# Kernel tuning notes

Measured on AMD Instinct MI355X. Metric: run time of the kernel, lower is better.

Reference implementation:

```python
import jax, jax.numpy as jnp
import numpy as np
import math

N = 50000      # nodes
E = 800000     # edges (avg degree 16)
T = 4          # time steps
F = 64         # feature dim (in = hidden = out)
MAX_LEN = 200  # positional encoding table length
EPS = 1e-5     # BatchNorm eps


def _make_pe(time_dim, max_len):
    pe = np.zeros((max_len, time_dim), dtype=np.float32)
    position = np.arange(max_len, dtype=np.float32)[:, None]
    div_term = np.exp(np.arange(0, time_dim, 2, dtype=np.float32) * (-math.log(10000.0) / time_dim))
    pe[:, 0::2] = np.sin(position * div_term)
    pe[:, 1::2] = np.cos(position * div_term)
    return jnp.asarray(pe)


def setup_inputs() -> dict:
    key = jax.random.key(0)
    ks = jax.random.split(key, 10)
    xav = math.sqrt(2.0 / (F + F))  # xavier_normal_ std for square linear
    return {
        "node_features": jax.random.normal(ks[0], (N, T, F), dtype=jnp.float32),
        "edges_weight": jax.random.uniform(ks[1], (T, E), dtype=jnp.float32),
        "identities": jax.random.randint(ks[2], (T,), 0, MAX_LEN),
        "edge_src": jax.random.randint(ks[3], (E,), 0, N),
        "edge_dst": jax.random.randint(ks[4], (E,), 0, N),
        "pe": _make_pe(F, MAX_LEN),
        "W0": jax.random.normal(ks[5], (F, F), dtype=jnp.float32) * xav,
        "W1": jax.random.normal(ks[6], (F, F), dtype=jnp.float32) * xav,
        "g0": jnp.ones((F,), jnp.float32),
        "b0": jnp.zeros((F,), jnp.float32),
        "g1": jnp.ones((F,), jnp.float32),
        "b1": jnp.zeros((F,), jnp.float32),
    }


def _gcn_layer(h, ew, edge_src, edge_dst, W):
    # gather-mul-scatter: msg_e = h[src_e] * w_e ; agg_v = sum_{e: dst=v} msg_e
    msg = h[edge_src] * ew                                   # (E, T, F)
    agg = jax.ops.segment_sum(msg, edge_dst, num_segments=N)  # (N, T, F)
    readout = agg.mean(axis=0)                                # dgl.mean_nodes (single graph) -> (T, F)
    return agg @ W, readout @ W


def _batchnorm(x, gamma, beta):
    # training-mode batch stats over all non-channel dims
    mean = x.mean(axis=(0, 1))
    var = x.var(axis=(0, 1))
    return (x - mean) * jax.lax.rsqrt(var + EPS) * gamma + beta


def reference(node_features, edges_weight, identities, edge_src, edge_dst,
              pe, W0, W1, g0, b0, g1, b1):
    # positional encoding added per time step
    h = node_features + pe[identities]          # (N, T, F)
    ew = edges_weight.T[:, :, None]             # (E, T, 1)
    # layer 0: gcn -> dropout(eval=identity) -> BN -> ReLU
    h, readout = _gcn_layer(h, ew, edge_src, edge_dst, W0)
    h = jax.nn.relu(_batchnorm(h, g0, b0))
    # layer 1 (output layer)
    h, readout = _gcn_layer(h, ew, edge_src, edge_dst, W1)
    h = jax.nn.relu(_batchnorm(h, g1, b1))
    return h, readout
```

## Files before the change

kernel.cpp:

```cpp
#include <hip/hip_runtime.h>

#define TF 256

typedef __attribute__((ext_vector_type(8))) short short8;
typedef __attribute__((ext_vector_type(4))) float f32x4;
typedef __attribute__((ext_vector_type(4))) unsigned int uint4v;
typedef __attribute__((ext_vector_type(2))) unsigned int uint2v;

__device__ inline unsigned short f2bf(float x) {
  unsigned u = __float_as_uint(x);
  u += 0x7fffu + ((u >> 16) & 1u);
  return (unsigned short)(u >> 16);
}
__device__ inline unsigned pack2(unsigned short lo, unsigned short hi) {
  return (unsigned)lo | ((unsigned)hi << 16);
}
__device__ inline float bflo(unsigned u) { return __uint_as_float(u << 16); }
__device__ inline float bfhi(unsigned u) { return __uint_as_float(u & 0xffff0000u); }

__global__ void prep_hist_kernel(const float* __restrict__ x, const float* __restrict__ pe,
                                 const int* __restrict__ ids, uint2v* __restrict__ h0, int n4,
                                 const int* __restrict__ dst, int* __restrict__ indeg, int E) {
  const int gid = blockIdx.x * blockDim.x + threadIdx.x;
  const int stride = gridDim.x * blockDim.x;
  for (int i = gid; i < n4; i += stride) {
    int e0 = (i << 2) & (TF - 1);
    int t = e0 >> 6;
    int f4 = e0 & 63;
    f32x4 v = __builtin_nontemporal_load(&reinterpret_cast<const f32x4*>(x)[i]);
    const f32x4 p = *reinterpret_cast<const f32x4*>(&pe[ids[t] * 64 + f4]);
    uint2v o;
    o.x = pack2(f2bf(v.x + p.x), f2bf(v.y + p.y));
    o.y = pack2(f2bf(v.z + p.z), f2bf(v.w + p.w));
    h0[i] = o;
  }
  for (int e = gid; e < E; e += stride) {
    atomicAdd(&indeg[__builtin_nontemporal_load(&dst[e])], 1);
  }
}

__global__ __launch_bounds__(1024) void scan_part1(const int* __restrict__ indeg,
                                                   int* __restrict__ partials, int n) {
  __shared__ int wsum[16];
  const int tid = threadIdx.x;
  const int lane = tid & 63;
  const int wid = tid >> 6;
  int i = blockIdx.x * 1024 + tid;
  int s = (i < n) ? indeg[i] : 0;
  #pragma unroll
  for (int o = 1; o < 64; o <<= 1) s += __shfl_xor(s, o, 64);
  if (lane == 0) wsum[wid] = s;
  __syncthreads();
  if (tid == 0) {
    int acc = 0;
    #pragma unroll
    for (int w = 0; w < 16; ++w) acc += wsum[w];
    partials[blockIdx.x] = acc;
  }
}

__global__ __launch_bounds__(512) void scan2_wfrag_kernel(
    const int* __restrict__ partials, int* __restrict__ base, int* __restrict__ offsets,
    int nb, int n, const float* __restrict__ W0, const float* __restrict__ W1,
    short* __restrict__ wf0, short* __restrict__ wf1) {
  const int tid = threadIdx.x;
  if (tid < 64) {
    int v = (tid < nb) ? partials[tid] : 0;
    int s = v;
    #pragma unroll
    for (int o = 1; o < 64; o <<= 1) {
      int t = __shfl_up(s, o, 64);
      if (tid >= o) s += t;
    }
    if (tid < nb) base[tid] = s - v;
    if (tid == nb - 1) offsets[n] = s;
  }
  const int frag = tid >> 6, lane = tid & 63;
  const int c = frag >> 1, h = frag & 1;
  const int col = (c << 4) + (lane & 15);
  const int k0 = h * 32 + ((lane >> 4) << 3);
  short* o0 = wf0 + frag * 512 + lane * 8;
  short* o1 = wf1 + frag * 512 + lane * 8;
  #pragma unroll
  for (int i = 0; i < 8; ++i) {
    o0[i] = (short)f2bf(W0[(k0 + i) * 64 + col]);
    o1[i] = (short)f2bf(W1[(k0 + i) * 64 + col]);
  }
}

__global__ __launch_bounds__(1024) void scan_part3(const int* __restrict__ indeg,
                                                   const int* __restrict__ base,
                                                   int* __restrict__ offsets,
                                                   int* __restrict__ cursor, int n) {
  __shared__ int wsum[16];
  const int tid = threadIdx.x;
  const int lane = tid & 63;
  const int wid = tid >> 6;
  int i = blockIdx.x * 1024 + tid;
  int v = (i < n) ? indeg[i] : 0;
  int s = v;
  #pragma unroll
  for (int o = 1; o < 64; o <<= 1) {
    int t = __shfl_up(s, o, 64);
    if (lane >= o) s += t;
  }
  if (lane == 63) wsum[wid] = s;
  __syncthreads();
  if (tid == 0) {
    int acc = 0;
    #pragma unroll
    for (int w = 0; w < 16; ++w) { int t = wsum[w]; wsum[w] = acc; acc += t; }
  }
  __syncthreads();
  int excl = s - v + wsum[wid] + base[blockIdx.x];
  if (i < n) { offsets[i] = excl; cursor[i] = excl; }
}

__global__ void fill_kernel(const int* __restrict__ src, const int* __restrict__ dst,
                            const float* __restrict__ ew, int* __restrict__ cursor,
                            uint4v* __restrict__ csr_ent, int E) {
  int e = blockIdx.x * blockDim.x + threadIdx.x;
  if (e >= E) return;
  int d = __builtin_nontemporal_load(&dst[e]);
  int pos = atomicAdd(&cursor[d], 1);
  uint4v ent;
  ent.x = (unsigned)(__builtin_nontemporal_load(&src[e]) << 9);
  float w0 = __builtin_nontemporal_load(&ew[e]);
  float w1 = __builtin_nontemporal_load(&ew[(size_t)E + e]);
  float w2 = __builtin_nontemporal_load(&ew[2 * (size_t)E + e]);
  float w3 = __builtin_nontemporal_load(&ew[3 * (size_t)E + e]);
  ent.y = pack2(f2bf(w0), f2bf(w1));
  ent.z = pack2(f2bf(w2), f2bf(w3));
  ent.w = 0u;
  __builtin_nontemporal_store(ent, &csr_ent[pos]);
}

template <int LAYER>
__global__ __launch_bounds__(256) void aggregate_kernel(
    const char* __restrict__ h_base, const int* __restrict__ offsets,
    const uint4v* __restrict__ csr_ent,
    const float* __restrict__ red, const float* __restrict__ g,
    const float* __restrict__ b, float inv_count,
    uint4v* __restrict__ agg, int n_nodes) {
  __shared__ float s_sc[64], s_sh[64];
  const int tid = threadIdx.x;
  if (LAYER == 1) {
    if (tid < 64) {
      float sum = red[tid] + red[64 + tid] + red[128 + tid] + red[192 + tid];
      float mean = sum * inv_count;
      float var = red[256 + tid] * inv_count - mean * mean;
      float sc = g[tid] * rsqrtf(var + 1e-5f);
      s_sc[tid] = sc;
      s_sh[tid] = fmaf(-mean, sc, b[tid]);
    }
    __syncthreads();
  }
  const int lane = tid & 63;
  const int wid = tid >> 6;
  const int v = blockIdx.x * 4 + wid;
  if (v >= n_nodes) return;
  const int p = lane >> 5;
  const unsigned q = lane & 31;
  const unsigned qb = q << 4;
  const int tw = q >> 3;

  float sc[8], sh[8];
  if (LAYER == 1) {
    const int f0 = (q & 7) << 3;
    #pragma unroll
    for (int j = 0; j < 8; ++j) { sc[j] = s_sc[f0 + j]; sh[j] = s_sh[f0 + j]; }
  }

  float acc[8];
  #pragma unroll
  for (int j = 0; j < 8; ++j) acc[j] = 0.f;

  auto wext = [&](uint4v ent) -> float {
    unsigned word = (tw & 2) ? ent.z : ent.y;
    return (tw & 1) ? bfhi(word) : bflo(word);
  };
  auto body = [&](uint4v u, float w) {
    float x[8] = {bflo(u.x), bfhi(u.x), bflo(u.y), bfhi(u.y),
                  bflo(u.z), bfhi(u.z), bflo(u.w), bfhi(u.w)};
    #pragma unroll
    for (int j = 0; j < 8; ++j) {
      float t = x[j];
      if (LAYER == 1) t = fmaxf(0.f, fmaf(t, sc[j], sh[j]));
      acc[j] = fmaf(w, t, acc[j]);
    }
  };

  const int beg = offsets[v];
  const int end = offsets[v + 1];
  int i = beg;
  for (; i + 8 <= end; i += 8) {
    uint4v ent[4];
    #pragma unroll
    for (int c = 0; c < 4; ++c) ent[c] = csr_ent[i + 2 * c + p];
    uint4v row[4];
    #pragma unroll
    for (int c = 0; c < 4; ++c)
      row[c] = *reinterpret_cast<const uint4v*>(h_base + (ent[c].x + qb));
    #pragma unroll
    for (int c = 0; c < 4; ++c) body(row[c], wext(ent[c]));
  }
  for (; i + 2 <= end; i += 2) {
    const uint4v ent = csr_ent[i + p];
    const uint4v row = *reinterpret_cast<const uint4v*>(h_base + (ent.x + qb));
    body(row, wext(ent));
  }
  if (i < end) {
    const uint4v ent = csr_ent[i];
    const uint4v row = *reinterpret_cast<const uint4v*>(h_base + (ent.x + qb));
    body(row, p == 0 ? wext(ent) : 0.f);
  }

  #pragma unroll
  for (int j = 0; j < 8; ++j) acc[j] += __shfl_xor(acc[j], 32, 64);
  if (lane < 32) {
    uint4v o;
    o.x = pack2(f2bf(acc[0]), f2bf(acc[1]));
    o.y = pack2(f2bf(acc[2]), f2bf(acc[3]));
    o.z = pack2(f2bf(acc[4]), f2bf(acc[5]));
    o.w = pack2(f2bf(acc[6]), f2bf(acc[7]));
    __builtin_nontemporal_store(o, &agg[(size_t)v * 32 + q]);
  }
}

__global__ __launch_bounds__(256) void mfma_matmul_kernel(
    const unsigned short* __restrict__ aggb, const short* __restrict__ wf,
    unsigned short* __restrict__ y_bf, float* __restrict__ part, int R) {
  const int tid = threadIdx.x;
  const int lane = tid & 63;
  const int wid = tid >> 6;

  short8 bfr[8];
  #pragma unroll
  for (int g = 0; g < 8; ++g)
    bfr[g] = *reinterpret_cast<const short8*>(wf + g * 512 + lane * 8);

  f32x4 csum[4];
  float ssq[4];
  #pragma unroll
  for (int c = 0; c < 4; ++c) { csum[c] = (f32x4){0.f, 0.f, 0.f, 0.f}; ssq[c] = 0.f; }

  const int nrb = (R + 15) >> 4;
  const int k0 = (lane >> 4) << 3;
  for (int rb = blockIdx.x * 4 + wid; rb < nrb; rb += gridDim.x * 4) {
    const int base = rb << 4;
    const int row = base + (lane & 15);
    short8 a0 = (short8){0, 0, 0, 0, 0, 0, 0, 0};
    short8 a1 = a0;
    if (row < R) {
      const short8* ap = reinterpret_cast<const short8*>(aggb + (size_t)row * 64 + k0);
      a0 = __builtin_nontemporal_load(ap);
      a1 = __builtin_nontemporal_load(ap + 4);
    }
    f32x4 acc[4];
    #pragma unroll
    for (int c = 0; c < 4; ++c) {
      acc[c] = (f32x4){0.f, 0.f, 0.f, 0.f};
      acc[c] = __builtin_amdgcn_mfma_f32_16x16x32_bf16(a0, bfr[c * 2 + 0], acc[c], 0, 0, 0);
      acc[c] = __builtin_amdgcn_mfma_f32_16x16x32_bf16(a1, bfr[c * 2 + 1], acc[c], 0, 0, 0);
    }
    const int rbase = base + ((lane >> 4) << 2);
    #pragma unroll
    for (int c = 0; c < 4; ++c) {
      const int col = (c << 4) + (lane & 15);
      #pragma unroll
      for (int i = 0; i < 4; ++i) {
        const int r2 = rbase + i;
        if (r2 < R) {
          const float val = acc[c][i];
          y_bf[(size_t)r2 * 64 + col] = f2bf(val);
          csum[c][i] += val;
          ssq[c] += val * val;
        }
      }
    }
  }

  #pragma unroll
  for (int c = 0; c < 4; ++c) {
    #pragma unroll
    for (int i = 0; i < 4; ++i) {
      float v = csum[c][i];
      v += __shfl_xor(v, 16, 64);
      v += __shfl_xor(v, 32, 64);
      csum[c][i] = v;
    }
    float q = ssq[c];
    q += __shfl_xor(q, 16, 64);
    q += __shfl_xor(q, 32, 64);
    ssq[c] = q;
  }
  __shared__ float lcs[4][256];
  __shared__ float lsq[4][64];
  if (lane < 16) {
    #pragma unroll
    for (int c = 0; c < 4; ++c) {
      #pragma unroll
      for (int i = 0; i < 4; ++i) lcs[wid][i * 64 + (c << 4) + lane] = csum[c][i];
      lsq[wid][(c << 4) + lane] = ssq[c];
    }
  }
  __syncthreads();
  float s = lcs[0][tid] + lcs[1][tid] + lcs[2][tid] + lcs[3][tid];
  part[(size_t)blockIdx.x * 320 + tid] = s;
  if (tid < 64)
    part[(size_t)blockIdx.x * 320 + 256 + tid] =
        lsq[0][tid] + lsq[1][tid] + lsq[2][tid] + lsq[3][tid];
}

__global__ __launch_bounds__(1024) void reduce_part_kernel(const float* __restrict__ part,
                                                           float* __restrict__ red, int nblk) {
  __shared__ float lds[1024];
  const int tid = threadIdx.x;
  const int col = blockIdx.x * 16 + (tid & 15);
  const int r = tid >> 4;
  float s = 0.f;
  for (int bk = r; bk < nblk; bk += 64) s += part[(size_t)bk * 320 + col];
  lds[tid] = s;
  __syncthreads();
  #pragma unroll
  for (int off = 512; off >= 16; off >>= 1) {
    if (tid < off) lds[tid] += lds[tid + off];
    __syncthreads();
  }
  if (tid < 16) red[col] = lds[tid];
}

__global__ __launch_bounds__(256) void bn_relu_out_kernel(
    const uint4v* __restrict__ yb, const float* __restrict__ red,
    const float* __restrict__ g, const float* __restrict__ b, float inv_count,
    float* __restrict__ out_readout, float invN, f32x4* __restrict__ out, int n8) {
  __shared__ float s_sc[64], s_sh[64];
  const int tid = threadIdx.x;
  if (tid < 64) {
    float sum = red[tid] + red[64 + tid] + red[128 + tid] + red[192 + tid];
    float mean = sum * inv_count;
    float var = red[256 + tid] * inv_count - mean * mean;
    float sc = g[tid] * rsqrtf(var + 1e-5f);
    s_sc[tid] = sc;
    s_sh[tid] = fmaf(-mean, sc, b[tid]);
  }
  __syncthreads();
  if (blockIdx.x == 0) out_readout[tid] = red[tid] * invN;
  const int i = blockIdx.x * 256 + tid;
  if (i >= n8) return;
  const int f0 = (i & 7) << 3;
  uint4v u = __builtin_nontemporal_load(&yb[i]);
  float x[8] = {bflo(u.x), bfhi(u.x), bflo(u.y), bfhi(u.y),
                bflo(u.z), bfhi(u.z), bflo(u.w), bfhi(u.w)};
  f32x4 o0, o1;
  o0.x = fmaxf(0.f, fmaf(x[0], s_sc[f0 + 0], s_sh[f0 + 0]));
  o0.y = fmaxf(0.f, fmaf(x[1], s_sc[f0 + 1], s_sh[f0 + 1]));
  o0.z = fmaxf(0.f, fmaf(x[2], s_sc[f0 + 2], s_sh[f0 + 2]));
  o0.w = fmaxf(0.f, fmaf(x[3], s_sc[f0 + 3], s_sh[f0 + 3]));
  o1.x = fmaxf(0.f, fmaf(x[4], s_sc[f0 + 4], s_sh[f0 + 4]));
  o1.y = fmaxf(0.f, fmaf(x[5], s_sc[f0 + 5], s_sh[f0 + 5]));
  o1.z = fmaxf(0.f, fmaf(x[6], s_sc[f0 + 6], s_sh[f0 + 6]));
  o1.w = fmaxf(0.f, fmaf(x[7], s_sc[f0 + 7], s_sh[f0 + 7]));
  __builtin_nontemporal_store(o0, &out[i * 2 + 0]);
  __builtin_nontemporal_store(o1, &out[i * 2 + 1]);
}

extern "C" void kernel_launch(void* const* d_in, const int* in_sizes, int n_in,
                              void* d_out, int out_size, void* d_ws, size_t ws_size,
                              hipStream_t stream) {
  const float* node_features = (const float*)d_in[0];
  const float* edges_weight  = (const float*)d_in[1];
  const int*   identities    = (const int*)d_in[2];
  const int*   edge_src      = (const int*)d_in[3];
  const int*   edge_dst      = (const int*)d_in[4];
  const float* pe            = (const float*)d_in[5];
  const float* W0            = (const float*)d_in[6];
  const float* W1            = (const float*)d_in[7];
  const float* g0            = (const float*)d_in[8];
  const float* b0            = (const float*)d_in[9];
  const float* g1            = (const float*)d_in[10];
  const float* b1            = (const float*)d_in[11];

  const int T = in_sizes[2];
  const int E = in_sizes[3];
  const int F = in_sizes[8];
  const int N = in_sizes[0] / (T * F);
  const int R = N * T;

  float* out = (float*)d_out;
  float* out_h = out;
  float* out_readout = out + (size_t)N * T * F;

  char* ws = (char*)d_ws;
  size_t off = 0;
  auto alloc = [&](size_t bytes) -> void* {
    off = (off + 255) & ~(size_t)255;
    void* p = ws + off;
    off += bytes;
    return p;
  };
  int*    indeg    = (int*)alloc((size_t)N * sizeof(int));
  int*    partials = (int*)alloc(64 * sizeof(int));
  int*    base_    = (int*)alloc(64 * sizeof(int));
  int*    offsets  = (int*)alloc(((size_t)N + 1) * sizeof(int));
  int*    cursor   = (int*)alloc((size_t)N * sizeof(int));
  uint4v* csr_ent  = (uint4v*)alloc(((size_t)E + 16) * 16);
  unsigned short* h0b  = (unsigned short*)alloc((size_t)N * TF * 2);
  unsigned short* aggb = (unsigned short*)alloc((size_t)N * TF * 2);
  short* wf0 = (short*)alloc(8 * 512 * sizeof(short));
  short* wf1 = (short*)alloc(8 * 512 * sizeof(short));
  const int MMB = 512;
  float* mm_part = (float*)alloc((size_t)MMB * 320 * sizeof(float));
  float* red     = (float*)alloc(320 * sizeof(float));
  (void)ws_size;

  const int nb = (N + 1023) / 1024;
  const float invR = 1.0f / (float)R;

  (void)hipMemsetAsync(indeg, 0, (size_t)N * sizeof(int), stream);
  hipLaunchKernelGGL(prep_hist_kernel, dim3(2048), dim3(256), 0, stream,
                     node_features, pe, identities, (uint2v*)h0b, (N * TF) / 4,
                     edge_dst, indeg, E);
  hipLaunchKernelGGL(scan_part1, dim3(nb), dim3(1024), 0, stream, indeg, partials, N);
  hipLaunchKernelGGL(scan2_wfrag_kernel, dim3(1), dim3(512), 0, stream,
                     partials, base_, offsets, nb, N, W0, W1, wf0, wf1);
  hipLaunchKernelGGL(scan_part3, dim3(nb), dim3(1024), 0, stream, indeg, base_, offsets, cursor, N);
  hipLaunchKernelGGL(fill_kernel, dim3((E + 255) / 256), dim3(256), 0, stream,
                     edge_src, edge_dst, edges_weight, cursor, csr_ent, E);

  const int agg_blocks = (N + 3) / 4;

  hipLaunchKernelGGL((aggregate_kernel<0>), dim3(agg_blocks), dim3(256), 0, stream,
                     (const char*)h0b, offsets, csr_ent,
                     nullptr, nullptr, nullptr, 0.f, (uint4v*)aggb, N);
  hipLaunchKernelGGL(mfma_matmul_kernel, dim3(MMB), dim3(256), 0, stream,
                     aggb, wf0, h0b , mm_part, R);
  hipLaunchKernelGGL(reduce_part_kernel, dim3(20), dim3(1024), 0, stream, mm_part, red, MMB);

  hipLaunchKernelGGL((aggregate_kernel<1>), dim3(agg_blocks), dim3(256), 0, stream,
                     (const char*)h0b , offsets, csr_ent,
                     red, g0, b0, invR, (uint4v*)aggb, N);
  hipLaunchKernelGGL(mfma_matmul_kernel, dim3(MMB), dim3(256), 0, stream,
                     aggb, wf1, h0b , mm_part, R);
  hipLaunchKernelGGL(reduce_part_kernel, dim3(20), dim3(1024), 0, stream, mm_part, red, MMB);

  hipLaunchKernelGGL(bn_relu_out_kernel, dim3((R * 8 + 255) / 256), dim3(256), 0, stream,
                     (const uint4v*)h0b, red, g1, b1, invR,
                     out_readout, 1.0f / (float)N, (f32x4*)out_h, R * 8);
}
```

Measured before the change: 289.0 us.

## Fuse neighbor aggregation with MFMA matmul and BN statistics per layer

Merges the CSR gather-aggregate and the bf16 MFMA matmul into one persistent kernel. Each block aggregates four nodes into a double-buffered LDS tile, then multiplies that 16x64 tile by the weight fragments and accumulates the BatchNorm partial sums. This removes the global round trip of the aggregated buffer and one launch per layer. In exchange it adds a block barrier per group, so waves with short neighbor lists wait for the slowest wave, and the grid becomes a fixed persistent size with a launch-bounds occupancy hint.

Measured after the change: 287.2 us. Within noise of the previous version (-0.6%).

```diff
diff --git a/kernel.cpp b/kernel.cpp
--- a/kernel.cpp
+++ b/kernel.cpp
@@ -136,14 +136,17 @@
 }
 
 template <int LAYER>
-__global__ __launch_bounds__(256) void aggregate_kernel(
+__global__ __launch_bounds__(256, 6) void fused_agg_mm_kernel(
     const char* __restrict__ h_base, const int* __restrict__ offsets,
-    const uint4v* __restrict__ csr_ent,
+    const uint4v* __restrict__ csr_ent, const short* __restrict__ wf,
     const float* __restrict__ red, const float* __restrict__ g,
     const float* __restrict__ b, float inv_count,
-    uint4v* __restrict__ agg, int n_nodes) {
+    unsigned short* __restrict__ y_bf, float* __restrict__ part, int n_groups) {
+  __shared__ unsigned short tile[2][16][72];
   __shared__ float s_sc[64], s_sh[64];
   const int tid = threadIdx.x;
+  const int lane = tid & 63;
+  const int wid = tid >> 6;
   if (LAYER == 1) {
     if (tid < 64) {
       float sum = red[tid] + red[64 + tid] + red[128 + tid] + red[192 + tid];
@@ -155,161 +158,118 @@
     }
     __syncthreads();
   }
-  const int lane = tid & 63;
-  const int wid = tid >> 6;
-  const int v = blockIdx.x * 4 + wid;
-  if (v >= n_nodes) return;
+  const short8 bf0 = *reinterpret_cast<const short8*>(wf + (wid * 2 + 0) * 512 + lane * 8);
+  const short8 bf1 = *reinterpret_cast<const short8*>(wf + (wid * 2 + 1) * 512 + lane * 8);
+
   const int p = lane >> 5;
   const unsigned q = lane & 31;
   const unsigned qb = q << 4;
   const int tw = q >> 3;
 
-  float sc[8], sh[8];
+  float scv[8], shv[8];
   if (LAYER == 1) {
     const int f0 = (q & 7) << 3;
     #pragma unroll
-    for (int j = 0; j < 8; ++j) { sc[j] = s_sc[f0 + j]; sh[j] = s_sh[f0 + j]; }
-  }
-
-  float acc[8];
+    for (int j = 0; j < 8; ++j) { scv[j] = s_sc[f0 + j]; shv[j] = s_sh[f0 + j]; }
+  }
+
+  f32x4 csum = (f32x4){0.f, 0.f, 0.f, 0.f};
+  float ssq = 0.f;
+  int buf = 0;
+
+  for (int grp = blockIdx.x; grp < n_groups; grp += gridDim.x) {
+    const int v = grp * 4 + wid;
+    float acc[8];
+    #pragma unroll
+    for (int j = 0; j < 8; ++j) acc[j] = 0.f;
+
+    auto wext = [&](uint4v ent) -> float {
+      unsigned word = (tw & 2) ? ent.z : ent.y;
+      return (tw & 1) ? bfhi(word) : bflo(word);
+    };
+    auto body = [&](uint4v u, float w) {
+      float x[8] = {bflo(u.x), bfhi(u.x), bflo(u.y), bfhi(u.y),
+                    bflo(u.z), bfhi(u.z), bflo(u.w), bfhi(u.w)};
+      #pragma unroll
+      for (int j = 0; j < 8; ++j) {
+        float t = x[j];
+        if (LAYER == 1) t = fmaxf(0.f, fmaf(t, scv[j], shv[j]));
+        acc[j] = fmaf(w, t, acc[j]);
+      }
+    };
+
+    const int beg = offsets[v];
+    const int end = offsets[v + 1];
+    int i = beg;
+    for (; i + 8 <= end; i += 8) {
+      uint4v ent[4];
+      #pragma unroll
+      for (int c = 0; c < 4; ++c) ent[c] = csr_ent[i + 2 * c + p];
+      uint4v row[4];
+      #pragma unroll
+      for (int c = 0; c < 4; ++c)
+        row[c] = *reinterpret_cast<const uint4v*>(h_base + (ent[c].x + qb));
+      #pragma unroll
+      for (int c = 0; c < 4; ++c) body(row[c], wext(ent[c]));
+    }
+    for (; i + 2 <= end; i += 2) {
+      const uint4v ent = csr_ent[i + p];
+      const uint4v row = *reinterpret_cast<const uint4v*>(h_base + (ent.x + qb));
+      body(row, wext(ent));
+    }
+    if (i < end) {
+      const uint4v ent = csr_ent[i];
+      const uint4v row = *reinterpret_cast<const uint4v*>(h_base + (ent.x + qb));
+      body(row, p == 0 ? wext(ent) : 0.f);
+    }
+
+    #pragma unroll
+    for (int j = 0; j < 8; ++j) acc[j] += __shfl_xor(acc[j], 32, 64);
+    if (lane < 32) {
+      uint4v o;
+      o.x = pack2(f2bf(acc[0]), f2bf(acc[1]));
+      o.y = pack2(f2bf(acc[2]), f2bf(acc[3]));
+      o.z = pack2(f2bf(acc[4]), f2bf(acc[5]));
+      o.w = pack2(f2bf(acc[6]), f2bf(acc[7]));
+      *reinterpret_cast<uint4v*>(&tile[buf][wid * 4 + (q >> 3)][(q & 7) * 8]) = o;
+    }
+    __syncthreads();
+
+    const int r = lane & 15;
+    const int k0 = (lane >> 4) << 3;
+    const short8 a0 = *reinterpret_cast<const short8*>(&tile[buf][r][k0]);
+    const short8 a1 = *reinterpret_cast<const short8*>(&tile[buf][r][k0 + 32]);
+    f32x4 dacc = (f32x4){0.f, 0.f, 0.f, 0.f};
+    dacc = __builtin_amdgcn_mfma_f32_16x16x32_bf16(a0, bf0, dacc, 0, 0, 0);
+    dacc = __builtin_amdgcn_mfma_f32_16x16x32_bf16(a1, bf1, dacc, 0, 0, 0);
+    const int gbase = grp * 16 + ((lane >> 4) << 2);
+    const int col = (wid << 4) + (lane & 15);
+    #pragma unroll
+    for (int i2 = 0; i2 < 4; ++i2) {
+      const float val = dacc[i2];
+      y_bf[(size_t)(gbase + i2) * 64 + col] = f2bf(val);
+      csum[i2] += val;
+      ssq += val * val;
+    }
+    buf ^= 1;
+  }
+
   #pragma unroll
-  for (int j = 0; j < 8; ++j) acc[j] = 0.f;
-
-  auto wext = [&](uint4v ent) -> float {
-    unsigned word = (tw & 2) ? ent.z : ent.y;
-    return (tw & 1) ? bfhi(word) : bflo(word);
-  };
-  auto body = [&](uint4v u, float w) {
-    float x[8] = {bflo(u.x), bfhi(u.x), bflo(u.y), bfhi(u.y),
-                  bflo(u.z), bfhi(u.z), bflo(u.w), bfhi(u.w)};
-    #pragma unroll
-    for (int j = 0; j < 8; ++j) {
-      float t = x[j];
-      if (LAYER == 1) t = fmaxf(0.f, fmaf(t, sc[j], sh[j]));
-      acc[j] = fmaf(w, t, acc[j]);
-    }
-  };
-
-  const int beg = offsets[v];
-  const int end = offsets[v + 1];
-  int i = beg;
-  for (; i + 8 <= end; i += 8) {
-    uint4v ent[4];
-    #pragma unroll
-    for (int c = 0; c < 4; ++c) ent[c] = csr_ent[i + 2 * c + p];
-    uint4v row[4];
-    #pragma unroll
-    for (int c = 0; c < 4; ++c)
-      row[c] = *reinterpret_cast<const uint4v*>(h_base + (ent[c].x + qb));
-    #pragma unroll
-    for (int c = 0; c < 4; ++c) body(row[c], wext(ent[c]));
-  }
-  for (; i + 2 <= end; i += 2) {
-    const uint4v ent = csr_ent[i + p];
-    const uint4v row = *reinterpret_cast<const uint4v*>(h_base + (ent.x + qb));
-    body(row, wext(ent));
-  }
-  if (i < end) {
-    const uint4v ent = csr_ent[i];
-    const uint4v row = *reinterpret_cast<const uint4v*>(h_base + (ent.x + qb));
-    body(row, p == 0 ? wext(ent) : 0.f);
-  }
-
-  #pragma unroll
-  for (int j = 0; j < 8; ++j) acc[j] += __shfl_xor(acc[j], 32, 64);
-  if (lane < 32) {
-    uint4v o;
-    o.x = pack2(f2bf(acc[0]), f2bf(acc[1]));
-    o.y = pack2(f2bf(acc[2]), f2bf(acc[3]));
-    o.z = pack2(f2bf(acc[4]), f2bf(acc[5]));
-    o.w = pack2(f2bf(acc[6]), f2bf(acc[7]));
-    __builtin_nontemporal_store(o, &agg[(size_t)v * 32 + q]);
-  }
-}
-
-__global__ __launch_bounds__(256) void mfma_matmul_kernel(
-    const unsigned short* __restrict__ aggb, const short* __restrict__ wf,
-    unsigned short* __restrict__ y_bf, float* __restrict__ part, int R) {
-  const int tid = threadIdx.x;
-  const int lane = tid & 63;
-  const int wid = tid >> 6;
-
-  short8 bfr[8];
-  #pragma unroll
-  for (int g = 0; g < 8; ++g)
-    bfr[g] = *reinterpret_cast<const short8*>(wf + g * 512 + lane * 8);
-
-  f32x4 csum[4];
-  float ssq[4];
-  #pragma unroll
-  for (int c = 0; c < 4; ++c) { csum[c] = (f32x4){0.f, 0.f, 0.f, 0.f}; ssq[c] = 0.f; }
-
-  const int nrb = (R + 15) >> 4;
-  const int k0 = (lane >> 4) << 3;
-  for (int rb = blockIdx.x * 4 + wid; rb < nrb; rb += gridDim.x * 4) {
-    const int base = rb << 4;
-    const int row = base + (lane & 15);
-    short8 a0 = (short8){0, 0, 0, 0, 0, 0, 0, 0};
-    short8 a1 = a0;
-    if (row < R) {
-      const short8* ap = reinterpret_cast<const short8*>(aggb + (size_t)row * 64 + k0);
-      a0 = __builtin_nontemporal_load(ap);
-      a1 = __builtin_nontemporal_load(ap + 4);
-    }
-    f32x4 acc[4];
-    #pragma unroll
-    for (int c = 0; c < 4; ++c) {
-      acc[c] = (f32x4){0.f, 0.f, 0.f, 0.f};
-      acc[c] = __builtin_amdgcn_mfma_f32_16x16x32_bf16(a0, bfr[c * 2 + 0], acc[c], 0, 0, 0);
-      acc[c] = __builtin_amdgcn_mfma_f32_16x16x32_bf16(a1, bfr[c * 2 + 1], acc[c], 0, 0, 0);
-    }
-    const int rbase = base + ((lane >> 4) << 2);
-    #pragma unroll
-    for (int c = 0; c < 4; ++c) {
-      const int col = (c << 4) + (lane & 15);
-      #pragma unroll
-      for (int i = 0; i < 4; ++i) {
-        const int r2 = rbase + i;
-        if (r2 < R) {
-          const float val = acc[c][i];
-          y_bf[(size_t)r2 * 64 + col] = f2bf(val);
-          csum[c][i] += val;
-          ssq[c] += val * val;
-        }
-      }
-    }
-  }
-
-  #pragma unroll
-  for (int c = 0; c < 4; ++c) {
-    #pragma unroll
-    for (int i = 0; i < 4; ++i) {
-      float v = csum[c][i];
-      v += __shfl_xor(v, 16, 64);
-      v += __shfl_xor(v, 32, 64);
-      csum[c][i] = v;
-    }
-    float q = ssq[c];
-    q += __shfl_xor(q, 16, 64);
-    q += __shfl_xor(q, 32, 64);
-    ssq[c] = q;
-  }
-  __shared__ float lcs[4][256];
-  __shared__ float lsq[4][64];
+  for (int i2 = 0; i2 < 4; ++i2) {
+    float vv = csum[i2];
+    vv += __shfl_xor(vv, 16, 64);
+    vv += __shfl_xor(vv, 32, 64);
+    csum[i2] = vv;
+  }
+  float qq = ssq;
+  qq += __shfl_xor(qq, 16, 64);
+  qq += __shfl_xor(qq, 32, 64);
   if (lane < 16) {
     #pragma unroll
-    for (int c = 0; c < 4; ++c) {
-      #pragma unroll
-      for (int i = 0; i < 4; ++i) lcs[wid][i * 64 + (c << 4) + lane] = csum[c][i];
-      lsq[wid][(c << 4) + lane] = ssq[c];
-    }
-  }
-  __syncthreads();
-  float s = lcs[0][tid] + lcs[1][tid] + lcs[2][tid] + lcs[3][tid];
-  part[(size_t)blockIdx.x * 320 + tid] = s;
-  if (tid < 64)
-    part[(size_t)blockIdx.x * 320 + 256 + tid] =
-        lsq[0][tid] + lsq[1][tid] + lsq[2][tid] + lsq[3][tid];
+    for (int i2 = 0; i2 < 4; ++i2)
+      part[(size_t)blockIdx.x * 320 + i2 * 64 + (wid << 4) + lane] = csum[i2];
+    part[(size_t)blockIdx.x * 320 + 256 + (wid << 4) + lane] = qq;
+  }
 }
 
 __global__ __launch_bounds__(1024) void reduce_part_kernel(const float* __restrict__ part,
@@ -406,16 +366,17 @@
   int*    cursor   = (int*)alloc((size_t)N * sizeof(int));
   uint4v* csr_ent  = (uint4v*)alloc(((size_t)E + 16) * 16);
   unsigned short* h0b  = (unsigned short*)alloc((size_t)N * TF * 2);
-  unsigned short* aggb = (unsigned short*)alloc((size_t)N * TF * 2);
+  unsigned short* y0b  = (unsigned short*)alloc((size_t)N * TF * 2);
   short* wf0 = (short*)alloc(8 * 512 * sizeof(short));
   short* wf1 = (short*)alloc(8 * 512 * sizeof(short));
-  const int MMB = 512;
-  float* mm_part = (float*)alloc((size_t)MMB * 320 * sizeof(float));
+  const int FB = 1536;
+  float* mm_part = (float*)alloc((size_t)FB * 320 * sizeof(float));
   float* red     = (float*)alloc(320 * sizeof(float));
   (void)ws_size;
 
   const int nb = (N + 1023) / 1024;
   const float invR = 1.0f / (float)R;
+  const int n_groups = N / 4;
 
   (void)hipMemsetAsync(indeg, 0, (size_t)N * sizeof(int), stream);
   hipLaunchKernelGGL(prep_hist_kernel, dim3(2048), dim3(256), 0, stream,
@@ -428,21 +389,15 @@
   hipLaunchKernelGGL(fill_kernel, dim3((E + 255) / 256), dim3(256), 0, stream,
                      edge_src, edge_dst, edges_weight, cursor, csr_ent, E);
 
-  const int agg_blocks = (N + 3) / 4;
-
-  hipLaunchKernelGGL((aggregate_kernel<0>), dim3(agg_blocks), dim3(256), 0, stream,
-                     (const char*)h0b, offsets, csr_ent,
-                     nullptr, nullptr, nullptr, 0.f, (uint4v*)aggb, N);
-  hipLaunchKernelGGL(mfma_matmul_kernel, dim3(MMB), dim3(256), 0, stream,
-                     aggb, wf0, h0b , mm_part, R);
-  hipLaunchKernelGGL(reduce_part_kernel, dim3(20), dim3(1024), 0, stream, mm_part, red, MMB);
-
-  hipLaunchKernelGGL((aggregate_kernel<1>), dim3(agg_blocks), dim3(256), 0, stream,
-                     (const char*)h0b , offsets, csr_ent,
-                     red, g0, b0, invR, (uint4v*)aggb, N);
-  hipLaunchKernelGGL(mfma_matmul_kernel, dim3(MMB), dim3(256), 0, stream,
-                     aggb, wf1, h0b , mm_part, R);
-  hipLaunchKernelGGL(reduce_part_kernel, dim3(20), dim3(1024), 0, stream, mm_part, red, MMB);
+  hipLaunchKernelGGL((fused_agg_mm_kernel<0>), dim3(FB), dim3(256), 0, stream,
+                     (const char*)h0b, offsets, csr_ent, wf0,
+                     nullptr, nullptr, nullptr, 0.f, y0b, mm_part, n_groups);
+  hipLaunchKernelGGL(reduce_part_kernel, dim3(20), dim3(1024), 0, stream, mm_part, red, FB);
+
+  hipLaunchKernelGGL((fused_agg_mm_kernel<1>), dim3(FB), dim3(256), 0, stream,
+                     (const char*)y0b, offsets, csr_ent, wf1,
+                     red, g0, b0, invR, h0b , mm_part, n_groups);
+  hipLaunchKernelGGL(reduce_part_kernel, dim3(20), dim3(1024), 0, stream, mm_part, red, FB);
 
   hipLaunchKernelGGL(bn_relu_out_kernel, dim3((R * 8 + 255) / 256), dim3(256), 0, stream,
                      (const uint4v*)h0b, red, g1, b1, invR,
```
